# Performance work log

Measured on AMD Instinct MI355X. Metric: run time of the kernel, lower is better.

Reference implementation:

```python
import jax, jax.numpy as jnp
import numpy as np

N_NODES = 100000
N_EDGES = 1600000
DIM = 64


def setup_inputs() -> dict:
    key = jax.random.key(0)
    k1, k2, k3 = jax.random.split(key, 3)
    x = jax.random.normal(k1, (N_NODES, DIM), dtype=jnp.float32)
    edge_index = jax.random.randint(k2, (2, N_EDGES), 0, N_NODES, dtype=jnp.int64)
    W = jax.random.normal(k3, (DIM, DIM), dtype=jnp.float32) * (1.0 / np.sqrt(DIM))
    b = jnp.zeros((DIM,), dtype=jnp.float32)
    return {"x": x, "edge_index": edge_index, "W": W, "b": b}


def reference(x, edge_index, W, b):
    # GCNConv (PyG defaults): add self-loops, symmetric normalization,
    # linear transform, scatter-add aggregation, bias; then ReLU.
    N = x.shape[0]
    loop = jnp.arange(N, dtype=edge_index.dtype)
    row = jnp.concatenate([edge_index[0], loop])  # source nodes
    col = jnp.concatenate([edge_index[1], loop])  # target nodes
    ew = jnp.ones(row.shape[0], dtype=x.dtype)

    deg = jax.ops.segment_sum(ew, col, num_segments=N)  # [N]
    dinv = jnp.where(deg > 0, jax.lax.rsqrt(deg), 0.0)
    norm = dinv[row] * ew * dinv[col]  # [E+N]

    xw = x @ W.T  # [N, D] small GEMM
    msg = norm[:, None] * xw[row]  # gather + scale, [E+N, D]
    out = jax.ops.segment_sum(msg, col, num_segments=N) + b  # scatter-add
    return jax.nn.relu(out)
```

## Files before the change

### kernel.cpp

```cpp
#include <hip/hip_runtime.h>
#include <hip/hip_bf16.h>

#define N_NODES 100000
#define N_EDGES 1600000
#define DIM 64
#define NBUCK 782
#define BK_NODES 128
#define CAP 2560
#define HA_EPB 16384
#define HA_BLOCKS 98
#define GEMM_BLOCKS 1563

typedef unsigned int uint32;
typedef __attribute__((ext_vector_type(8))) short bf16x8;
typedef __attribute__((ext_vector_type(4))) float f32x4;

__device__ __forceinline__ float bflo(uint32 u) { return __uint_as_float(u << 16); }
__device__ __forceinline__ float bfhi(uint32 u) { return __uint_as_float(u & 0xffff0000u); }

__device__ __forceinline__ short f2bf(float f) {
    __hip_bfloat16 h = __float2bfloat16(f);
    return (short)__builtin_bit_cast(unsigned short, h);
}
__device__ __forceinline__ uint32 pack2bf(float lo, float hi) {
    unsigned short a = __builtin_bit_cast(unsigned short, __float2bfloat16(lo));
    unsigned short b = __builtin_bit_cast(unsigned short, __float2bfloat16(hi));
    return ((uint32)b << 16) | (uint32)a;
}

__global__ __launch_bounds__(1024) void scatter_kernel(const int* __restrict__ row,
                                                       const int* __restrict__ col,
                                                       int* __restrict__ bcnt,
                                                       int* __restrict__ pairs) {
    __shared__ int h[NBUCK];
    __shared__ int base[NBUCK];
    if (threadIdx.x < NBUCK) h[threadIdx.x] = 0;
    __syncthreads();

    const int bstart = blockIdx.x * HA_EPB;
    int r[16], c[16];
#pragma unroll 16
    for (int k = 0; k < 16; ++k) {
        int e = bstart + threadIdx.x + k * 1024;
        if (e < N_EDGES) {
            r[k] = row[e];
            c[k] = col[e];
            atomicAdd(&h[c[k] >> 7], 1);
        }
    }
    __syncthreads();
    if (threadIdx.x < NBUCK) {
        int v = h[threadIdx.x];
        base[threadIdx.x] = v ? atomicAdd(&bcnt[threadIdx.x], v) : 0;
        h[threadIdx.x] = 0;
    }
    __syncthreads();
#pragma unroll 16
    for (int k = 0; k < 16; ++k) {
        int e = bstart + threadIdx.x + k * 1024;
        if (e < N_EDGES) {
            int bk = c[k] >> 7;
            int pos = base[bk] + atomicAdd(&h[bk], 1);
            if (pos < CAP) pairs[bk * CAP + pos] = (r[k] << 7) | (c[k] & 127);
        }
    }
}

struct SortSmem {
    int cnt[BK_NODES];
    int sc[BK_NODES];
    int cur[BK_NODES];
    int buf[CAP];
};
union FusedSmem {
    SortSmem s;
    float g[64 * 64];
};

__global__ __launch_bounds__(256) void sortgemm_kernel(const int* __restrict__ bcnt,
                                                       int* __restrict__ pairs,
                                                       int* __restrict__ info,
                                                       float* __restrict__ dinv,
                                                       const float* __restrict__ x,
                                                       const float* __restrict__ W,
                                                       uint32* __restrict__ sbw) {
    __shared__ FusedSmem u;
    const int tid = threadIdx.x;

    if (blockIdx.x < NBUCK) {
        const int b = blockIdx.x;
        int n = bcnt[b];
        if (n > CAP) n = CAP;
        if (tid < BK_NODES) u.s.cnt[tid] = 0;
        __syncthreads();
        for (int p = tid; p < n; p += 256) {
            int pk = pairs[b * CAP + p];
            u.s.buf[p] = pk;
            atomicAdd(&u.s.cnt[pk & 127], 1);
        }
        __syncthreads();
        if (tid < BK_NODES) {
            int lane = tid & 63;
            int sum = u.s.cnt[tid];
#pragma unroll
            for (int d = 1; d < 64; d <<= 1) {
                int t = __shfl_up(sum, d);
                if (lane >= d) sum += t;
            }
            u.s.sc[tid] = sum;
        }
        __syncthreads();
        if (tid >= 64 && tid < BK_NODES) u.s.sc[tid] += u.s.sc[63];
        __syncthreads();
        if (tid < BK_NODES) {
            int ex = u.s.sc[tid] - u.s.cnt[tid];
            u.s.cur[tid] = ex;
            int node = b * BK_NODES + tid;
            if (node < N_NODES) {
                info[node] = ((b * CAP + ex) << 8) | u.s.cnt[tid];
                dinv[node] = rsqrtf((float)(u.s.cnt[tid] + 1));
            }
        }
        __syncthreads();
        for (int p = tid; p < n; p += 256) {
            int pk = u.s.buf[p];
            int pos = atomicAdd(&u.s.cur[pk & 127], 1);
            pairs[b * CAP + pos] = pk >> 7;
        }
    } else {
        const int wave = tid >> 6;
        const int lane = tid & 63;
        const int base = (blockIdx.x - NBUCK) * 64;
        const int r16 = lane & 15;
        const int kb = lane >> 4;

        bf16x8 wb[4][2];
#pragma unroll
        for (int t = 0; t < 4; ++t) {
#pragma unroll
            for (int h = 0; h < 2; ++h) {
                const float* wp = &W[(r16 + 16 * t) * DIM + 32 * h + kb * 8];
                float4 p0 = *(const float4*)wp;
                float4 p1 = *(const float4*)(wp + 4);
                bf16x8 f;
                f[0] = f2bf(p0.x); f[1] = f2bf(p0.y); f[2] = f2bf(p0.z); f[3] = f2bf(p0.w);
                f[4] = f2bf(p1.x); f[5] = f2bf(p1.y); f[6] = f2bf(p1.z); f[7] = f2bf(p1.w);
                wb[t][h] = f;
            }
        }

        int arow = base + wave * 16 + r16;
        if (arow >= N_NODES) arow = N_NODES - 1;
        bf16x8 af[2];
#pragma unroll
        for (int h = 0; h < 2; ++h) {
            const float* xp = &x[(size_t)arow * DIM + 32 * h + kb * 8];
            float4 p0 = *(const float4*)xp;
            float4 p1 = *(const float4*)(xp + 4);
            bf16x8 f;
            f[0] = f2bf(p0.x); f[1] = f2bf(p0.y); f[2] = f2bf(p0.z); f[3] = f2bf(p0.w);
            f[4] = f2bf(p1.x); f[5] = f2bf(p1.y); f[6] = f2bf(p1.z); f[7] = f2bf(p1.w);
            af[h] = f;
        }

#pragma unroll
        for (int t = 0; t < 4; ++t) {
            f32x4 c = {0.0f, 0.0f, 0.0f, 0.0f};
            c = __builtin_amdgcn_mfma_f32_16x16x32_bf16(af[0], wb[t][0], c, 0, 0, 0);
            c = __builtin_amdgcn_mfma_f32_16x16x32_bf16(af[1], wb[t][1], c, 0, 0, 0);
#pragma unroll
            for (int i = 0; i < 4; ++i)
                u.g[(wave * 16 + kb * 4 + i) * 64 + r16 + 16 * t] = c[i];
        }
        __syncthreads();

        int r = tid >> 2;
        int cb = tid & 3;
        int nrow = base + r;
        if (nrow < N_NODES) {
            const float* src = &u.g[r * 64 + cb * 16];
            uint32 o[8];
#pragma unroll
            for (int j = 0; j < 8; ++j) {
                float2 f = *(const float2*)&src[2 * j];
                o[j] = pack2bf(f.x, f.y);
            }
            uint32* dst = sbw + (size_t)nrow * 32 + cb * 8;
            *(uint4*)dst = make_uint4(o[0], o[1], o[2], o[3]);
            *(uint4*)(dst + 4) = make_uint4(o[4], o[5], o[6], o[7]);
        }
    }
}

__global__ __launch_bounds__(256) void agg_kernel(const int* __restrict__ info,
                                                  const int* __restrict__ srow,
                                                  const uint2* __restrict__ s4,
                                                  const float* __restrict__ dinv,
                                                  const float* __restrict__ bias,
                                                  float* __restrict__ out) {
    int n = __builtin_amdgcn_readfirstlane(blockIdx.x * 4 + (threadIdx.x >> 6));
    if (n >= N_NODES) return;
    const int lane = threadIdx.x & 63;
    const int q = lane >> 4;
    const int l = lane & 15;

    const int iv = info[n];
    const int start = iv >> 8;
    const int end = start + (iv & 255);

    float a0 = 0.0f, a1 = 0.0f, a2 = 0.0f, a3 = 0.0f;
    int p = start + q;
    for (; p + 12 < end; p += 16) {
        int r0 = srow[p];
        int r1 = srow[p + 4];
        int r2 = srow[p + 8];
        int r3 = srow[p + 12];
        float d0 = dinv[r0], d1 = dinv[r1], d2 = dinv[r2], d3 = dinv[r3];
        uint2 u0 = s4[(size_t)r0 * 16 + l];
        uint2 u1 = s4[(size_t)r1 * 16 + l];
        uint2 u2 = s4[(size_t)r2 * 16 + l];
        uint2 u3 = s4[(size_t)r3 * 16 + l];
        a0 = fmaf(d0, bflo(u0.x), a0); a1 = fmaf(d0, bfhi(u0.x), a1);
        a2 = fmaf(d0, bflo(u0.y), a2); a3 = fmaf(d0, bfhi(u0.y), a3);
        a0 = fmaf(d1, bflo(u1.x), a0); a1 = fmaf(d1, bfhi(u1.x), a1);
        a2 = fmaf(d1, bflo(u1.y), a2); a3 = fmaf(d1, bfhi(u1.y), a3);
        a0 = fmaf(d2, bflo(u2.x), a0); a1 = fmaf(d2, bfhi(u2.x), a1);
        a2 = fmaf(d2, bflo(u2.y), a2); a3 = fmaf(d2, bfhi(u2.y), a3);
        a0 = fmaf(d3, bflo(u3.x), a0); a1 = fmaf(d3, bfhi(u3.x), a1);
        a2 = fmaf(d3, bflo(u3.y), a2); a3 = fmaf(d3, bfhi(u3.y), a3);
    }
    for (; p < end; p += 4) {
        int r0 = srow[p];
        float d0 = dinv[r0];
        uint2 u0 = s4[(size_t)r0 * 16 + l];
        a0 = fmaf(d0, bflo(u0.x), a0); a1 = fmaf(d0, bfhi(u0.x), a1);
        a2 = fmaf(d0, bflo(u0.y), a2); a3 = fmaf(d0, bfhi(u0.y), a3);
    }

    a0 += __shfl_xor(a0, 16); a1 += __shfl_xor(a1, 16);
    a2 += __shfl_xor(a2, 16); a3 += __shfl_xor(a3, 16);
    a0 += __shfl_xor(a0, 32); a1 += __shfl_xor(a1, 32);
    a2 += __shfl_xor(a2, 32); a3 += __shfl_xor(a3, 32);

    if (lane < 16) {
        float dc = dinv[n];
        uint2 us = s4[(size_t)n * 16 + l];
        a0 = fmaf(dc, bflo(us.x), a0); a1 = fmaf(dc, bfhi(us.x), a1);
        a2 = fmaf(dc, bflo(us.y), a2); a3 = fmaf(dc, bfhi(us.y), a3);
        float4 bb = *(const float4*)&bias[4 * l];
        f32x4 o;
        o[0] = fmaxf(fmaf(dc, a0, bb.x), 0.0f);
        o[1] = fmaxf(fmaf(dc, a1, bb.y), 0.0f);
        o[2] = fmaxf(fmaf(dc, a2, bb.z), 0.0f);
        o[3] = fmaxf(fmaf(dc, a3, bb.w), 0.0f);
        __builtin_nontemporal_store(o, (f32x4*)&out[(size_t)n * DIM + 4 * l]);
    }
}

extern "C" void kernel_launch(void* const* d_in, const int* in_sizes, int n_in,
                              void* d_out, int out_size, void* d_ws, size_t ws_size,
                              hipStream_t stream) {
    const float* x    = (const float*)d_in[0];
    const int*   ei   = (const int*)d_in[1];
    const float* W    = (const float*)d_in[2];
    const float* bias = (const float*)d_in[3];
    float*       out  = (float*)d_out;

    const int* row = ei;
    const int* col = ei + N_EDGES;

    char* ws = (char*)d_ws;
    int*    bcnt  = (int*)(ws + 0);
    int*    info  = (int*)(ws + 4096);
    float*  dinv  = (float*)(ws + 404224);
    int*    pairs = (int*)(ws + 804352);
    uint32* sbw   = (uint32*)(ws + 8812160);

    hipMemsetAsync(bcnt, 0, 4096, stream);
    scatter_kernel<<<HA_BLOCKS, 1024, 0, stream>>>(row, col, bcnt, pairs);
    sortgemm_kernel<<<NBUCK + GEMM_BLOCKS, 256, 0, stream>>>(bcnt, pairs, info, dinv,
                                                             x, W, sbw);
    agg_kernel<<<(N_NODES + 3) / 4, 256, 0, stream>>>(info, pairs, (const uint2*)sbw,
                                                      dinv, bias, out);
}
```

Baseline: 103.9 us.

## Fold source-side normalization into GEMM output and compute degrees via global atomics

Node in-degrees are now counted with global atomics in the scatter kernel, so the per-bucket sort no longer does shared-memory histogramming. The GEMM epilogue scales each transformed row by its own dinv before storing it as bf16, so the aggregation kernel only sums gathered rows and drops the per-edge dinv gather. This trades 1.6M global atomics and a wider memset for fewer random loads in the aggregation. Rounding changes slightly because the scale is applied before bf16 conversion.

```diff
diff --git a/kernel.cpp b/kernel.cpp
--- a/kernel.cpp
+++ b/kernel.cpp
@@ -31,6 +31,7 @@
 __global__ __launch_bounds__(1024) void scatter_kernel(const int* __restrict__ row,
                                                        const int* __restrict__ col,
                                                        int* __restrict__ bcnt,
+                                                       int* __restrict__ deg,
                                                        int* __restrict__ pairs) {
     __shared__ int h[NBUCK];
     __shared__ int base[NBUCK];
@@ -46,6 +47,7 @@
             r[k] = row[e];
             c[k] = col[e];
             atomicAdd(&h[c[k] >> 7], 1);
+            atomicAdd(&deg[c[k]], 1);
         }
     }
     __syncthreads();
@@ -78,9 +80,9 @@
 };
 
 __global__ __launch_bounds__(256) void sortgemm_kernel(const int* __restrict__ bcnt,
+                                                       const int* __restrict__ deg,
                                                        int* __restrict__ pairs,
                                                        int* __restrict__ info,
-                                                       float* __restrict__ dinv,
                                                        const float* __restrict__ x,
                                                        const float* __restrict__ W,
                                                        uint32* __restrict__ sbw) {
@@ -91,13 +93,12 @@
         const int b = blockIdx.x;
         int n = bcnt[b];
         if (n > CAP) n = CAP;
-        if (tid < BK_NODES) u.s.cnt[tid] = 0;
-        __syncthreads();
-        for (int p = tid; p < n; p += 256) {
-            int pk = pairs[b * CAP + p];
-            u.s.buf[p] = pk;
-            atomicAdd(&u.s.cnt[pk & 127], 1);
-        }
+        if (tid < BK_NODES) {
+            int node = b * BK_NODES + tid;
+            u.s.cnt[tid] = (node < N_NODES) ? deg[node] : 0;
+        }
+        for (int p = tid; p < n; p += 256)
+            u.s.buf[p] = pairs[b * CAP + p];
         __syncthreads();
         if (tid < BK_NODES) {
             int lane = tid & 63;
@@ -116,10 +117,8 @@
             int ex = u.s.sc[tid] - u.s.cnt[tid];
             u.s.cur[tid] = ex;
             int node = b * BK_NODES + tid;
-            if (node < N_NODES) {
+            if (node < N_NODES)
                 info[node] = ((b * CAP + ex) << 8) | u.s.cnt[tid];
-                dinv[node] = rsqrtf((float)(u.s.cnt[tid] + 1));
-            }
         }
         __syncthreads();
         for (int p = tid; p < n; p += 256) {
@@ -163,6 +162,13 @@
             af[h] = f;
         }
 
+        float dv[4];
+#pragma unroll
+        for (int i = 0; i < 4; ++i) {
+            int rr = base + wave * 16 + kb * 4 + i;
+            dv[i] = rsqrtf((float)(deg[rr < N_NODES ? rr : N_NODES - 1] + 1));
+        }
+
 #pragma unroll
         for (int t = 0; t < 4; ++t) {
             f32x4 c = {0.0f, 0.0f, 0.0f, 0.0f};
@@ -170,7 +176,7 @@
             c = __builtin_amdgcn_mfma_f32_16x16x32_bf16(af[1], wb[t][1], c, 0, 0, 0);
 #pragma unroll
             for (int i = 0; i < 4; ++i)
-                u.g[(wave * 16 + kb * 4 + i) * 64 + r16 + 16 * t] = c[i];
+                u.g[(wave * 16 + kb * 4 + i) * 64 + r16 + 16 * t] = c[i] * dv[i];
         }
         __syncthreads();
 
@@ -195,7 +201,7 @@
 __global__ __launch_bounds__(256) void agg_kernel(const int* __restrict__ info,
                                                   const int* __restrict__ srow,
                                                   const uint2* __restrict__ s4,
-                                                  const float* __restrict__ dinv,
+                                                  const int* __restrict__ deg,
                                                   const float* __restrict__ bias,
                                                   float* __restrict__ out) {
     int n = __builtin_amdgcn_readfirstlane(blockIdx.x * 4 + (threadIdx.x >> 6));
@@ -215,26 +221,19 @@
         int r1 = srow[p + 4];
         int r2 = srow[p + 8];
         int r3 = srow[p + 12];
-        float d0 = dinv[r0], d1 = dinv[r1], d2 = dinv[r2], d3 = dinv[r3];
         uint2 u0 = s4[(size_t)r0 * 16 + l];
         uint2 u1 = s4[(size_t)r1 * 16 + l];
         uint2 u2 = s4[(size_t)r2 * 16 + l];
         uint2 u3 = s4[(size_t)r3 * 16 + l];
-        a0 = fmaf(d0, bflo(u0.x), a0); a1 = fmaf(d0, bfhi(u0.x), a1);
-        a2 = fmaf(d0, bflo(u0.y), a2); a3 = fmaf(d0, bfhi(u0.y), a3);
-        a0 = fmaf(d1, bflo(u1.x), a0); a1 = fmaf(d1, bfhi(u1.x), a1);
-        a2 = fmaf(d1, bflo(u1.y), a2); a3 = fmaf(d1, bfhi(u1.y), a3);
-        a0 = fmaf(d2, bflo(u2.x), a0); a1 = fmaf(d2, bfhi(u2.x), a1);
-        a2 = fmaf(d2, bflo(u2.y), a2); a3 = fmaf(d2, bfhi(u2.y), a3);
-        a0 = fmaf(d3, bflo(u3.x), a0); a1 = fmaf(d3, bfhi(u3.x), a1);
-        a2 = fmaf(d3, bflo(u3.y), a2); a3 = fmaf(d3, bfhi(u3.y), a3);
+        a0 += bflo(u0.x); a1 += bfhi(u0.x); a2 += bflo(u0.y); a3 += bfhi(u0.y);
+        a0 += bflo(u1.x); a1 += bfhi(u1.x); a2 += bflo(u1.y); a3 += bfhi(u1.y);
+        a0 += bflo(u2.x); a1 += bfhi(u2.x); a2 += bflo(u2.y); a3 += bfhi(u2.y);
+        a0 += bflo(u3.x); a1 += bfhi(u3.x); a2 += bflo(u3.y); a3 += bfhi(u3.y);
     }
     for (; p < end; p += 4) {
         int r0 = srow[p];
-        float d0 = dinv[r0];
         uint2 u0 = s4[(size_t)r0 * 16 + l];
-        a0 = fmaf(d0, bflo(u0.x), a0); a1 = fmaf(d0, bfhi(u0.x), a1);
-        a2 = fmaf(d0, bflo(u0.y), a2); a3 = fmaf(d0, bfhi(u0.y), a3);
+        a0 += bflo(u0.x); a1 += bfhi(u0.x); a2 += bflo(u0.y); a3 += bfhi(u0.y);
     }
 
     a0 += __shfl_xor(a0, 16); a1 += __shfl_xor(a1, 16);
@@ -243,10 +242,9 @@
     a2 += __shfl_xor(a2, 32); a3 += __shfl_xor(a3, 32);
 
     if (lane < 16) {
-        float dc = dinv[n];
+        float dc = rsqrtf((float)(deg[n] + 1));
         uint2 us = s4[(size_t)n * 16 + l];
-        a0 = fmaf(dc, bflo(us.x), a0); a1 = fmaf(dc, bfhi(us.x), a1);
-        a2 = fmaf(dc, bflo(us.y), a2); a3 = fmaf(dc, bfhi(us.y), a3);
+        a0 += bflo(us.x); a1 += bfhi(us.x); a2 += bflo(us.y); a3 += bfhi(us.y);
         float4 bb = *(const float4*)&bias[4 * l];
         f32x4 o;
         o[0] = fmaxf(fmaf(dc, a0, bb.x), 0.0f);
@@ -271,15 +269,15 @@
 
     char* ws = (char*)d_ws;
     int*    bcnt  = (int*)(ws + 0);
-    int*    info  = (int*)(ws + 4096);
-    float*  dinv  = (float*)(ws + 404224);
+    int*    deg   = (int*)(ws + 4096);
+    int*    info  = (int*)(ws + 404224);
     int*    pairs = (int*)(ws + 804352);
     uint32* sbw   = (uint32*)(ws + 8812160);
 
-    hipMemsetAsync(bcnt, 0, 4096, stream);
-    scatter_kernel<<<HA_BLOCKS, 1024, 0, stream>>>(row, col, bcnt, pairs);
-    sortgemm_kernel<<<NBUCK + GEMM_BLOCKS, 256, 0, stream>>>(bcnt, pairs, info, dinv,
+    hipMemsetAsync(ws, 0, 404096, stream);
+    scatter_kernel<<<HA_BLOCKS, 1024, 0, stream>>>(row, col, bcnt, deg, pairs);
+    sortgemm_kernel<<<NBUCK + GEMM_BLOCKS, 256, 0, stream>>>(bcnt, deg, pairs, info,
                                                              x, W, sbw);
     agg_kernel<<<(N_NODES + 3) / 4, 256, 0, stream>>>(info, pairs, (const uint2*)sbw,
-                                                      dinv, bias, out);
-}
+                                                      deg, bias, out);
+}
```

After: 161.5 us. +55.5%, slower.
